# Kernel optimization log

Measured on AMD Instinct MI355X. Metric: run time of the kernel, lower is better.

Reference implementation:

```python
import jax, jax.numpy as jnp
import numpy as np
from jax.scipy.special import logsumexp

N, K, D = 131072, 256, 32


def setup_inputs() -> dict:
    key = jax.random.key(0)
    k1, k2, k3 = jax.random.split(key, 3)
    points = jax.random.normal(k1, (N, D), dtype=jnp.float32)
    centers = jax.random.uniform(k2, (K, D), dtype=jnp.float32)
    # well-conditioned inverse-sqrt covariances (original used 15*I; scaled to
    # avoid float32 overflow in sqrt(det(covs_inv)) for D=32)
    covs_inv_sqrt = (0.5 * jnp.broadcast_to(jnp.eye(D, dtype=jnp.float32), (K, D, D))
                     + 0.02 * jax.random.normal(k3, (K, D, D), dtype=jnp.float32))
    weights = jnp.ones((K,), dtype=jnp.float32)
    threshold = jnp.zeros((1,), dtype=jnp.float32)
    return {"points": points, "centers": centers,
            "covs_inv_sqrt": covs_inv_sqrt, "weights": weights,
            "threshold": threshold}


def reference(points, centers, covs_inv_sqrt, weights, threshold):
    # refresh(): equal_clusters=True branch
    w = jnp.abs(weights)
    center_prs = w / (w.sum() + 1e-30)                       # [K]
    covs_inv = jnp.einsum('kde,kfe->kdf', covs_inv_sqrt, covs_inv_sqrt)  # [K,D,D]
    coefs = center_prs * jnp.sqrt(jnp.linalg.det(covs_inv))  # [K]

    # pairwise weighted sqdist: q_ij = (x_i - c_j)^T A_j (x_i - c_j)
    B = covs_inv.reshape(K, D * D)                           # [K, D*D]
    X2 = (points[:, :, None] * points[:, None, :]).reshape(N, D * D)  # [N, D*D]
    t_xAx = X2 @ B.T                                         # [N, K]
    m = jnp.einsum('kde,ke->kd', covs_inv, centers)          # A_j c_j, [K,D]
    t_xAc = points @ m.T                                     # [N, K]
    t_cAc = jnp.einsum('kd,kd->k', m, centers)               # [K]
    d_ij = -0.5 * (t_xAx - 2.0 * t_xAc + t_cAc[None, :])     # [N, K]

    # weighted logsumexp over centers, then subtract threshold
    ll = logsumexp(d_ij, axis=1, b=coefs[None, :])           # [N]
    return ll[:, None] - threshold[0]                        # [N, 1]
```

## Files before the change

kernel.cpp:

```cpp
#include <hip/hip_runtime.h>
#include <math.h>

#define NPTS 131072
#define KCOMP 256
#define DIM 32
#define NREAL 560
#define NCH 18
#define PSIF_BYTES 294912
#define WS_NEED (PSIF_BYTES + KCOMP * 4)

typedef __attribute__((ext_vector_type(8))) short short8;
typedef __attribute__((ext_vector_type(16))) float f32x16;

__device__ __forceinline__ unsigned short f2bf(float v) {
    unsigned u = __float_as_uint(v);
    u += 0x7fffu + ((u >> 16) & 1u);
    return (unsigned short)(u >> 16);
}

__device__ __forceinline__ unsigned pkbf(float lo, float hi) {
#if __has_builtin(__builtin_amdgcn_perm)
    const unsigned a = __float_as_uint(hi) + 0x8000u;
    const unsigned b = __float_as_uint(lo) + 0x8000u;
    return __builtin_amdgcn_perm(a, b, 0x07060302u);
#else
    return (unsigned)f2bf(lo) | ((unsigned)f2bf(hi) << 16);
#endif
}

__device__ __forceinline__ void dma16(const uint4* g, uint4* s) {
    __builtin_amdgcn_global_load_lds(
        (const __attribute__((address_space(1))) void*)g,
        (__attribute__((address_space(3))) void*)s, 16, 0, 0);
}

template<int N>
__device__ __forceinline__ void waitbar() {
    if constexpr (N == 2)
        asm volatile("s_waitcnt vmcnt(2) lgkmcnt(0)\ns_barrier" ::: "memory");
    else if constexpr (N == 1)
        asm volatile("s_waitcnt vmcnt(1) lgkmcnt(0)\ns_barrier" ::: "memory");
    else
        asm volatile("s_waitcnt vmcnt(0) lgkmcnt(0)\ns_barrier" ::: "memory");
}

constexpr int PfxT(int d) { return 32 * d - (d * (d - 1)) / 2; }
constexpr int rowT(int p) { int d = 0; while (d < 31 && PfxT(d + 1) <= p) ++d; return d; }
constexpr int colT(int p) { return rowT(p) + (p - PfxT(rowT(p))); }

template<int P, int J>
__device__ __forceinline__ float genOne(const float (&x)[DIM]) {
    constexpr int p = P + J;
    if constexpr (p >= NREAL) {
        return 0.f;
    } else if constexpr (p >= 528) {
        return x[p - 528];
    } else {
        constexpr int d = rowT(p);
        constexpr int f = colT(p);
        static_assert(d >= 0 && d < 32 && f >= d && f < 32, "bad feature map");
        return x[d] * x[f];
    }
}

__global__ __launch_bounds__(256) void gmm_pre(
    const float* __restrict__ S,
    const float* __restrict__ centers,
    const float* __restrict__ weights,
    unsigned short* __restrict__ PsiF,
    float* __restrict__ kc2)
{
    __shared__ float Sl[DIM][DIM + 1];
    __shared__ float As[DIM][DIM + 1];
    __shared__ float cl[DIM], ml[DIM];
    __shared__ float red[256];

    const int k = blockIdx.x, tid = threadIdx.x;

    for (int idx = tid; idx < DIM * DIM; idx += 256)
        Sl[idx >> 5][idx & 31] = S[(size_t)k * DIM * DIM + idx];
    if (tid < DIM) cl[tid] = centers[k * DIM + tid];
    __syncthreads();

    for (int idx = tid; idx < DIM * DIM; idx += 256) {
        const int d = idx >> 5, f = idx & 31;
        float a = 0.f;
#pragma unroll
        for (int e = 0; e < DIM; ++e) a = fmaf(Sl[d][e], Sl[f][e], a);
        As[d][f] = a;
    }
    __syncthreads();

    if (tid < DIM) {
        float mv = 0.f;
#pragma unroll
        for (int f = 0; f < DIM; ++f) mv = fmaf(As[tid][f], cl[f], mv);
        ml[tid] = mv;
    }
    __syncthreads();

    for (int p = tid; p < NREAL; p += 256) {
        float val;
        if (p < 528) {
            int d = 0, pr = 0;
            while (pr + (32 - d) <= p) { pr += (32 - d); ++d; }
            const int f = d + (p - pr);
            val = (f == d) ? -0.5f * As[d][d] : -As[d][f];
        } else {
            val = ml[p - 528];
        }
        const int c = p >> 6, kk = p & 63;
        const int s = kk >> 4, qq = (kk >> 3) & 1, j = kk & 7;
        const int ct = k >> 5, ll = qq * 32 + (k & 31);
        const int g = c * 2048 + (s * 8 + ct) * 64 + ll;
        PsiF[(size_t)g * 8 + j] = f2bf(val);
    }

    red[tid] = fabsf(weights[tid]);
    __syncthreads();
    for (int off = 128; off > 0; off >>= 1) {
        if (tid < off) red[tid] += red[tid + off];
        __syncthreads();
    }
    const float wsum = red[0];

    for (int j = 0; j < DIM - 1; ++j) {
        const float inv = 1.0f / As[j][j];
        for (int idx = tid; idx < DIM * DIM; idx += 256) {
            const int r = idx >> 5, c = idx & 31;
            if (r > j && c > j)
                As[r][c] = fmaf(-As[r][j] * inv, As[j][c], As[r][c]);
        }
        __syncthreads();
    }

    if (tid < DIM) red[tid] = __logf(As[tid][tid]);
    __syncthreads();
    if (tid == 0) {
        float sl = 0.f;
        for (int j = 0; j < DIM; ++j) sl += red[j];
        float cac = 0.f;
        for (int d2 = 0; d2 < DIM; ++d2) cac = fmaf(ml[d2], cl[d2], cac);
        kc2[k] = __logf(fabsf(weights[k])) - __logf(wsum + 1e-30f)
               + 0.5f * sl - 0.5f * cac;
    }
}

template<int P>
__device__ __forceinline__ void genQuad(const float (&x)[DIM], float* v) {
    v[0] = genOne<P, 0>(x);
    v[1] = genOne<P, 1>(x);
    v[2] = genOne<P, 2>(x);
    v[3] = genOne<P, 3>(x);
}

template<int CH, int SS>
__device__ __forceinline__ void genSite(const float (&x)[DIM], uint4* base,
                                        int rbg, int r32) {
    float v[8];
    genQuad<CH * 32 + SS * 8>(x, v);
    genQuad<CH * 32 + SS * 8 + 4>(x, v + 4);
    uint4 u;
    u.x = pkbf(v[0], v[1]);
    u.y = pkbf(v[2], v[3]);
    u.z = pkbf(v[4], v[5]);
    u.w = pkbf(v[6], v[7]);
    base[(SS >> 1) * 256 + rbg * 64 + (SS & 1) * 32 + r32] = u;
}

template<int CH>
__device__ __forceinline__ void genChunk(const float (&x)[DIM], uint4* sA4,
                                         int q, int rbg, int r32) {
    uint4* base = sA4 + (CH & 1) * 512;
    if constexpr (CH < 17) {
        if (q == 0)      genSite<CH, 0>(x, base, rbg, r32);
        else if (q == 1) genSite<CH, 1>(x, base, rbg, r32);
        else if (q == 2) genSite<CH, 2>(x, base, rbg, r32);
        else             genSite<CH, 3>(x, base, rbg, r32);
    } else {
        if (q == 0)      genSite<CH, 0>(x, base, rbg, r32);
        else if (q == 1) genSite<CH, 1>(x, base, rbg, r32);
    }
}

template<int C>
__device__ __forceinline__ void doChunk(const float (&x)[DIM],
    uint4* sA4, uint4* sB4, const uint4* __restrict__ PsiF4,
    f32x16 (&acc)[2][2],
    int l, int w, int q, int rbg, int r32, int rgp, int cgp)
{

    if constexpr (C + 2 < NCH) {
        constexpr int NI = (C + 2 == 17) ? 1 : 2;
        const uint4* src = PsiF4 + (C + 2) * 1024 + w * 64 + l;
        uint4* dst = sB4 + ((C + 2) % 3) * 1024 + w * 64 + l;
#pragma unroll
        for (int i = 0; i < NI; ++i) dma16(src + i * 512, dst + i * 512);
    }

    if constexpr (C + 1 < NCH) genChunk<C + 1>(x, sA4, q, rbg, r32);

    constexpr int NS = (C < 17) ? 2 : 1;
    const uint4* aa = sA4 + (C & 1) * 512;
    const uint4* bb = sB4 + (C % 3) * 1024;
#pragma unroll
    for (int s = 0; s < NS; ++s) {
        short8 f0 = __builtin_bit_cast(short8, aa[(s * 4 + rgp * 2 + 0) * 64 + l]);
        short8 f1 = __builtin_bit_cast(short8, aa[(s * 4 + rgp * 2 + 1) * 64 + l]);
#pragma unroll
        for (int cj = 0; cj < 2; ++cj) {
            short8 psi = __builtin_bit_cast(short8, bb[(s * 8 + cgp * 2 + cj) * 64 + l]);
            acc[0][cj] = __builtin_amdgcn_mfma_f32_32x32x16_bf16(psi, f0, acc[0][cj], 0, 0, 0);
            acc[1][cj] = __builtin_amdgcn_mfma_f32_32x32x16_bf16(psi, f1, acc[1][cj], 0, 0, 0);
        }
    }

    if constexpr (C <= 14)      waitbar<2>();
    else if constexpr (C == 15) waitbar<1>();
    else if constexpr (C == 16) waitbar<0>();
}

__global__ __launch_bounds__(512, 4) void gmm_mfma(
    const float* __restrict__ points,
    const unsigned short* __restrict__ PsiF,
    const float* __restrict__ kc2,
    const float* __restrict__ thr,
    float* __restrict__ out)
{
    __shared__ uint4 sA4[1024];
    __shared__ uint4 sB4[3072];
    float (*sM)[4] = (float (*)[4])sA4;
    float (*sS)[4] = (float (*)[4])(sA4 + 128);

    const int t = threadIdx.x;
    const int w = t >> 6, l = t & 63;
    const int row = t & 127, q = t >> 7;
    const int rbg = row >> 5, r32 = row & 31;
    const int rgp = w >> 2, cgp = w & 3;

    const uint4* PsiF4 = (const uint4*)PsiF;

    {
        const uint4* src = PsiF4 + w * 64 + l;
        uint4* dst = sB4 + w * 64 + l;
        dma16(src,        dst);
        dma16(src +  512, dst +  512);
        dma16(src + 1024, dst + 1024);
        dma16(src + 1536, dst + 1536);
    }

    float x[DIM];
    const float4* px = (const float4*)(points + ((size_t)blockIdx.x * 128 + row) * DIM);
#pragma unroll
    for (int j2 = 0; j2 < 8; ++j2) {
        float4 v = px[j2];
        x[4 * j2 + 0] = v.x; x[4 * j2 + 1] = v.y;
        x[4 * j2 + 2] = v.z; x[4 * j2 + 3] = v.w;
    }

    f32x16 acc[2][2];
#pragma unroll
    for (int ri = 0; ri < 2; ++ri)
#pragma unroll
        for (int cj = 0; cj < 2; ++cj)
#pragma unroll
            for (int r = 0; r < 16; ++r) acc[ri][cj][r] = 0.f;

    genChunk<0>(x, sA4, q, rbg, r32);
    __syncthreads();

    doChunk<0>(x, sA4, sB4, PsiF4, acc, l, w, q, rbg, r32, rgp, cgp);
    doChunk<1>(x, sA4, sB4, PsiF4, acc, l, w, q, rbg, r32, rgp, cgp);
    doChunk<2>(x, sA4, sB4, PsiF4, acc, l, w, q, rbg, r32, rgp, cgp);
    doChunk<3>(x, sA4, sB4, PsiF4, acc, l, w, q, rbg, r32, rgp, cgp);
    doChunk<4>(x, sA4, sB4, PsiF4, acc, l, w, q, rbg, r32, rgp, cgp);
    doChunk<5>(x, sA4, sB4, PsiF4, acc, l, w, q, rbg, r32, rgp, cgp);
    doChunk<6>(x, sA4, sB4, PsiF4, acc, l, w, q, rbg, r32, rgp, cgp);
    doChunk<7>(x, sA4, sB4, PsiF4, acc, l, w, q, rbg, r32, rgp, cgp);
    doChunk<8>(x, sA4, sB4, PsiF4, acc, l, w, q, rbg, r32, rgp, cgp);
    doChunk<9>(x, sA4, sB4, PsiF4, acc, l, w, q, rbg, r32, rgp, cgp);
    doChunk<10>(x, sA4, sB4, PsiF4, acc, l, w, q, rbg, r32, rgp, cgp);
    doChunk<11>(x, sA4, sB4, PsiF4, acc, l, w, q, rbg, r32, rgp, cgp);
    doChunk<12>(x, sA4, sB4, PsiF4, acc, l, w, q, rbg, r32, rgp, cgp);
    doChunk<13>(x, sA4, sB4, PsiF4, acc, l, w, q, rbg, r32, rgp, cgp);
    doChunk<14>(x, sA4, sB4, PsiF4, acc, l, w, q, rbg, r32, rgp, cgp);
    doChunk<15>(x, sA4, sB4, PsiF4, acc, l, w, q, rbg, r32, rgp, cgp);
    doChunk<16>(x, sA4, sB4, PsiF4, acc, l, w, q, rbg, r32, rgp, cgp);
    doChunk<17>(x, sA4, sB4, PsiF4, acc, l, w, q, rbg, r32, rgp, cgp);

    const int hi = l >> 5;
    float mr[2] = { -INFINITY, -INFINITY };
#pragma unroll
    for (int cj = 0; cj < 2; ++cj) {
        const float* kp = kc2 + (cgp * 2 + cj) * 32 + 4 * hi;
        const float4 q0 = *(const float4*)(kp);
        const float4 q1 = *(const float4*)(kp + 8);
        const float4 q2 = *(const float4*)(kp + 16);
        const float4 q3 = *(const float4*)(kp + 24);
#pragma unroll
        for (int ri = 0; ri < 2; ++ri) {
#define KADD(R, QC) { float _v = acc[ri][cj][R] + (QC); acc[ri][cj][R] = _v; mr[ri] = fmaxf(mr[ri], _v); }
            KADD(0, q0.x)  KADD(1, q0.y)  KADD(2, q0.z)  KADD(3, q0.w)
            KADD(4, q1.x)  KADD(5, q1.y)  KADD(6, q1.z)  KADD(7, q1.w)
            KADD(8, q2.x)  KADD(9, q2.y)  KADD(10, q2.z) KADD(11, q2.w)
            KADD(12, q3.x) KADD(13, q3.y) KADD(14, q3.z) KADD(15, q3.w)
#undef KADD
        }
    }
#pragma unroll
    for (int ri = 0; ri < 2; ++ri) {
        float m = fmaxf(mr[ri], __shfl_xor(mr[ri], 32, 64));
        float sv = 0.f;
#pragma unroll
        for (int cj = 0; cj < 2; ++cj)
#pragma unroll
            for (int rg = 0; rg < 16; ++rg)
                sv += __expf(acc[ri][cj][rg] - m);
        sv += __shfl_xor(sv, 32, 64);
        if (l < 32) {
            sM[(rgp * 2 + ri) * 32 + l][cgp] = m;
            sS[(rgp * 2 + ri) * 32 + l][cgp] = sv;
        }
    }
    __syncthreads();

    if (t < 128) {
        const float m0 = sM[t][0], m1 = sM[t][1], m2 = sM[t][2], m3 = sM[t][3];
        const float M = fmaxf(fmaxf(m0, m1), fmaxf(m2, m3));
        const float Sv = sS[t][0] * __expf(m0 - M) + sS[t][1] * __expf(m1 - M)
                       + sS[t][2] * __expf(m2 - M) + sS[t][3] * __expf(m3 - M);
        out[(size_t)blockIdx.x * 128 + t] = M + __logf(Sv) - thr[0];
    }
}

extern "C" void kernel_launch(void* const* d_in, const int* in_sizes, int n_in,
                              void* d_out, int out_size, void* d_ws, size_t ws_size,
                              hipStream_t stream) {
    const float* points  = (const float*)d_in[0];
    const float* centers = (const float*)d_in[1];
    const float* covs    = (const float*)d_in[2];
    const float* weights = (const float*)d_in[3];
    const float* thr     = (const float*)d_in[4];
    float* out = (float*)d_out;

    unsigned short* PsiF = (unsigned short*)d_ws;
    float* kc2 = (float*)((char*)d_ws + PSIF_BYTES);

    gmm_pre<<<KCOMP, 256, 0, stream>>>(covs, centers, weights, PsiF, kc2);
    gmm_mfma<<<NPTS / 128, 512, 0, stream>>>(points, PsiF, kc2, thr, out);
}
```

Baseline: 130.2 us.

## Load Psi fragments directly into registers and shrink blocks to 64 points

```diff
diff --git a/kernel.cpp b/kernel.cpp
--- a/kernel.cpp
+++ b/kernel.cpp
@@ -28,20 +28,8 @@
 #endif
 }
 
-__device__ __forceinline__ void dma16(const uint4* g, uint4* s) {
-    __builtin_amdgcn_global_load_lds(
-        (const __attribute__((address_space(1))) void*)g,
-        (__attribute__((address_space(3))) void*)s, 16, 0, 0);
-}
-
-template<int N>
-__device__ __forceinline__ void waitbar() {
-    if constexpr (N == 2)
-        asm volatile("s_waitcnt vmcnt(2) lgkmcnt(0)\ns_barrier" ::: "memory");
-    else if constexpr (N == 1)
-        asm volatile("s_waitcnt vmcnt(1) lgkmcnt(0)\ns_barrier" ::: "memory");
-    else
-        asm volatile("s_waitcnt vmcnt(0) lgkmcnt(0)\ns_barrier" ::: "memory");
+__device__ __forceinline__ void barrier_lds() {
+    asm volatile("s_waitcnt lgkmcnt(0)\ns_barrier" ::: "memory");
 }
 
 constexpr int PfxT(int d) { return 32 * d - (d * (d - 1)) / 2; }
@@ -155,8 +143,7 @@
 }
 
 template<int CH, int SS>
-__device__ __forceinline__ void genSite(const float (&x)[DIM], uint4* base,
-                                        int rbg, int r32) {
+__device__ __forceinline__ void genSiteW(const float (&x)[DIM], uint4* sA4, int l) {
     float v[8];
     genQuad<CH * 32 + SS * 8>(x, v);
     genQuad<CH * 32 + SS * 8 + 4>(x, v + 4);
@@ -165,92 +152,82 @@
     u.y = pkbf(v[2], v[3]);
     u.z = pkbf(v[4], v[5]);
     u.w = pkbf(v[6], v[7]);
-    base[(SS >> 1) * 256 + rbg * 64 + (SS & 1) * 32 + r32] = u;
+    uint4* base = sA4 + (CH & 1) * 256;
+    base[(((SS >> 1) * 2 + (l >> 5)) << 6) + (SS & 1) * 32 + (l & 31)] = u;
 }
 
 template<int CH>
-__device__ __forceinline__ void genChunk(const float (&x)[DIM], uint4* sA4,
-                                         int q, int rbg, int r32) {
-    uint4* base = sA4 + (CH & 1) * 512;
+__device__ __forceinline__ void genChunkW(const float (&x)[DIM], uint4* sA4,
+                                          int w, int l) {
     if constexpr (CH < 17) {
-        if (q == 0)      genSite<CH, 0>(x, base, rbg, r32);
-        else if (q == 1) genSite<CH, 1>(x, base, rbg, r32);
-        else if (q == 2) genSite<CH, 2>(x, base, rbg, r32);
-        else             genSite<CH, 3>(x, base, rbg, r32);
+        if      (w == 0) genSiteW<CH, 0>(x, sA4, l);
+        else if (w == 1) genSiteW<CH, 1>(x, sA4, l);
+        else if (w == 2) genSiteW<CH, 2>(x, sA4, l);
+        else             genSiteW<CH, 3>(x, sA4, l);
     } else {
-        if (q == 0)      genSite<CH, 0>(x, base, rbg, r32);
-        else if (q == 1) genSite<CH, 1>(x, base, rbg, r32);
+        if      (w == 0) genSiteW<CH, 0>(x, sA4, l);
+        else if (w == 1) genSiteW<CH, 1>(x, sA4, l);
+    }
+}
+
+template<int C>
+__device__ __forceinline__ void loadB(const uint4* __restrict__ PsiF4,
+                                      uint4 (&st)[4], int l, int cgp) {
+    const uint4* p = PsiF4 + C * 1024 + (cgp * 2) * 64 + l;
+    st[0] = p[0];
+    st[1] = p[64];
+    if constexpr (C < 17) {
+        st[2] = p[512];
+        st[3] = p[512 + 64];
     }
 }
 
 template<int C>
 __device__ __forceinline__ void doChunk(const float (&x)[DIM],
-    uint4* sA4, uint4* sB4, const uint4* __restrict__ PsiF4,
-    f32x16 (&acc)[2][2],
-    int l, int w, int q, int rbg, int r32, int rgp, int cgp)
+    uint4* sA4, const uint4* __restrict__ PsiF4,
+    uint4 (&cur)[4], uint4 (&nxt)[4],
+    f32x16 (&acc)[2][2], int l, int w)
 {
 
-    if constexpr (C + 2 < NCH) {
-        constexpr int NI = (C + 2 == 17) ? 1 : 2;
-        const uint4* src = PsiF4 + (C + 2) * 1024 + w * 64 + l;
-        uint4* dst = sB4 + ((C + 2) % 3) * 1024 + w * 64 + l;
-#pragma unroll
-        for (int i = 0; i < NI; ++i) dma16(src + i * 512, dst + i * 512);
-    }
-
-    if constexpr (C + 1 < NCH) genChunk<C + 1>(x, sA4, q, rbg, r32);
+    if constexpr (C + 1 < NCH) loadB<C + 1>(PsiF4, nxt, l, w);
+
+    if constexpr (C + 1 < NCH) genChunkW<C + 1>(x, sA4, w, l);
 
     constexpr int NS = (C < 17) ? 2 : 1;
-    const uint4* aa = sA4 + (C & 1) * 512;
-    const uint4* bb = sB4 + (C % 3) * 1024;
-#pragma unroll
-    for (int s = 0; s < NS; ++s) {
-        short8 f0 = __builtin_bit_cast(short8, aa[(s * 4 + rgp * 2 + 0) * 64 + l]);
-        short8 f1 = __builtin_bit_cast(short8, aa[(s * 4 + rgp * 2 + 1) * 64 + l]);
+    const uint4* aa = sA4 + (C & 1) * 256;
+#pragma unroll
+    for (int s2 = 0; s2 < NS; ++s2) {
+        short8 f0 = __builtin_bit_cast(short8, aa[(s2 * 2 + 0) * 64 + l]);
+        short8 f1 = __builtin_bit_cast(short8, aa[(s2 * 2 + 1) * 64 + l]);
 #pragma unroll
         for (int cj = 0; cj < 2; ++cj) {
-            short8 psi = __builtin_bit_cast(short8, bb[(s * 8 + cgp * 2 + cj) * 64 + l]);
+            short8 psi = __builtin_bit_cast(short8, cur[s2 * 2 + cj]);
             acc[0][cj] = __builtin_amdgcn_mfma_f32_32x32x16_bf16(psi, f0, acc[0][cj], 0, 0, 0);
             acc[1][cj] = __builtin_amdgcn_mfma_f32_32x32x16_bf16(psi, f1, acc[1][cj], 0, 0, 0);
         }
     }
 
-    if constexpr (C <= 14)      waitbar<2>();
-    else if constexpr (C == 15) waitbar<1>();
-    else if constexpr (C == 16) waitbar<0>();
-}
-
-__global__ __launch_bounds__(512, 4) void gmm_mfma(
+    if constexpr (C + 1 < NCH) barrier_lds();
+}
+
+__global__ __launch_bounds__(256, 3) void gmm_mfma(
     const float* __restrict__ points,
     const unsigned short* __restrict__ PsiF,
     const float* __restrict__ kc2,
     const float* __restrict__ thr,
     float* __restrict__ out)
 {
-    __shared__ uint4 sA4[1024];
-    __shared__ uint4 sB4[3072];
-    float (*sM)[4] = (float (*)[4])sA4;
-    float (*sS)[4] = (float (*)[4])(sA4 + 128);
+    __shared__ uint4 sA4[512];
+    __shared__ float sM[64][4];
+    __shared__ float sS[64][4];
 
     const int t = threadIdx.x;
     const int w = t >> 6, l = t & 63;
-    const int row = t & 127, q = t >> 7;
-    const int rbg = row >> 5, r32 = row & 31;
-    const int rgp = w >> 2, cgp = w & 3;
 
     const uint4* PsiF4 = (const uint4*)PsiF;
 
-    {
-        const uint4* src = PsiF4 + w * 64 + l;
-        uint4* dst = sB4 + w * 64 + l;
-        dma16(src,        dst);
-        dma16(src +  512, dst +  512);
-        dma16(src + 1024, dst + 1024);
-        dma16(src + 1536, dst + 1536);
-    }
-
     float x[DIM];
-    const float4* px = (const float4*)(points + ((size_t)blockIdx.x * 128 + row) * DIM);
+    const float4* px = (const float4*)(points + ((size_t)blockIdx.x * 64 + l) * DIM);
 #pragma unroll
     for (int j2 = 0; j2 < 8; ++j2) {
         float4 v = px[j2];
@@ -266,33 +243,36 @@
 #pragma unroll
             for (int r = 0; r < 16; ++r) acc[ri][cj][r] = 0.f;
 
-    genChunk<0>(x, sA4, q, rbg, r32);
-    __syncthreads();
-
-    doChunk<0>(x, sA4, sB4, PsiF4, acc, l, w, q, rbg, r32, rgp, cgp);
-    doChunk<1>(x, sA4, sB4, PsiF4, acc, l, w, q, rbg, r32, rgp, cgp);
-    doChunk<2>(x, sA4, sB4, PsiF4, acc, l, w, q, rbg, r32, rgp, cgp);
-    doChunk<3>(x, sA4, sB4, PsiF4, acc, l, w, q, rbg, r32, rgp, cgp);
-    doChunk<4>(x, sA4, sB4, PsiF4, acc, l, w, q, rbg, r32, rgp, cgp);
-    doChunk<5>(x, sA4, sB4, PsiF4, acc, l, w, q, rbg, r32, rgp, cgp);
-    doChunk<6>(x, sA4, sB4, PsiF4, acc, l, w, q, rbg, r32, rgp, cgp);
-    doChunk<7>(x, sA4, sB4, PsiF4, acc, l, w, q, rbg, r32, rgp, cgp);
-    doChunk<8>(x, sA4, sB4, PsiF4, acc, l, w, q, rbg, r32, rgp, cgp);
-    doChunk<9>(x, sA4, sB4, PsiF4, acc, l, w, q, rbg, r32, rgp, cgp);
-    doChunk<10>(x, sA4, sB4, PsiF4, acc, l, w, q, rbg, r32, rgp, cgp);
-    doChunk<11>(x, sA4, sB4, PsiF4, acc, l, w, q, rbg, r32, rgp, cgp);
-    doChunk<12>(x, sA4, sB4, PsiF4, acc, l, w, q, rbg, r32, rgp, cgp);
-    doChunk<13>(x, sA4, sB4, PsiF4, acc, l, w, q, rbg, r32, rgp, cgp);
-    doChunk<14>(x, sA4, sB4, PsiF4, acc, l, w, q, rbg, r32, rgp, cgp);
-    doChunk<15>(x, sA4, sB4, PsiF4, acc, l, w, q, rbg, r32, rgp, cgp);
-    doChunk<16>(x, sA4, sB4, PsiF4, acc, l, w, q, rbg, r32, rgp, cgp);
-    doChunk<17>(x, sA4, sB4, PsiF4, acc, l, w, q, rbg, r32, rgp, cgp);
+    uint4 stA[4], stB[4];
+    loadB<0>(PsiF4, stA, l, w);
+
+    genChunkW<0>(x, sA4, w, l);
+    barrier_lds();
+
+    doChunk<0>(x, sA4, PsiF4, stA, stB, acc, l, w);
+    doChunk<1>(x, sA4, PsiF4, stB, stA, acc, l, w);
+    doChunk<2>(x, sA4, PsiF4, stA, stB, acc, l, w);
+    doChunk<3>(x, sA4, PsiF4, stB, stA, acc, l, w);
+    doChunk<4>(x, sA4, PsiF4, stA, stB, acc, l, w);
+    doChunk<5>(x, sA4, PsiF4, stB, stA, acc, l, w);
+    doChunk<6>(x, sA4, PsiF4, stA, stB, acc, l, w);
+    doChunk<7>(x, sA4, PsiF4, stB, stA, acc, l, w);
+    doChunk<8>(x, sA4, PsiF4, stA, stB, acc, l, w);
+    doChunk<9>(x, sA4, PsiF4, stB, stA, acc, l, w);
+    doChunk<10>(x, sA4, PsiF4, stA, stB, acc, l, w);
+    doChunk<11>(x, sA4, PsiF4, stB, stA, acc, l, w);
+    doChunk<12>(x, sA4, PsiF4, stA, stB, acc, l, w);
+    doChunk<13>(x, sA4, PsiF4, stB, stA, acc, l, w);
+    doChunk<14>(x, sA4, PsiF4, stA, stB, acc, l, w);
+    doChunk<15>(x, sA4, PsiF4, stB, stA, acc, l, w);
+    doChunk<16>(x, sA4, PsiF4, stA, stB, acc, l, w);
+    doChunk<17>(x, sA4, PsiF4, stB, stA, acc, l, w);
 
     const int hi = l >> 5;
     float mr[2] = { -INFINITY, -INFINITY };
 #pragma unroll
     for (int cj = 0; cj < 2; ++cj) {
-        const float* kp = kc2 + (cgp * 2 + cj) * 32 + 4 * hi;
+        const float* kp = kc2 + (w * 2 + cj) * 32 + 4 * hi;
         const float4 q0 = *(const float4*)(kp);
         const float4 q1 = *(const float4*)(kp + 8);
         const float4 q2 = *(const float4*)(kp + 16);
@@ -318,18 +298,18 @@
                 sv += __expf(acc[ri][cj][rg] - m);
         sv += __shfl_xor(sv, 32, 64);
         if (l < 32) {
-            sM[(rgp * 2 + ri) * 32 + l][cgp] = m;
-            sS[(rgp * 2 + ri) * 32 + l][cgp] = sv;
-        }
-    }
-    __syncthreads();
-
-    if (t < 128) {
+            sM[ri * 32 + l][w] = m;
+            sS[ri * 32 + l][w] = sv;
+        }
+    }
+    __syncthreads();
+
+    if (t < 64) {
         const float m0 = sM[t][0], m1 = sM[t][1], m2 = sM[t][2], m3 = sM[t][3];
         const float M = fmaxf(fmaxf(m0, m1), fmaxf(m2, m3));
         const float Sv = sS[t][0] * __expf(m0 - M) + sS[t][1] * __expf(m1 - M)
                        + sS[t][2] * __expf(m2 - M) + sS[t][3] * __expf(m3 - M);
-        out[(size_t)blockIdx.x * 128 + t] = M + __logf(Sv) - thr[0];
+        out[(size_t)blockIdx.x * 64 + t] = M + __logf(Sv) - thr[0];
     }
 }
 
@@ -347,5 +327,5 @@
     float* kc2 = (float*)((char*)d_ws + PSIF_BYTES);
 
     gmm_pre<<<KCOMP, 256, 0, stream>>>(covs, centers, weights, PsiF, kc2);
-    gmm_mfma<<<NPTS / 128, 512, 0, stream>>>(points, PsiF, kc2, thr, out);
-}
+    gmm_mfma<<<NPTS / 64, 256, 0, stream>>>(points, PsiF, kc2, thr, out);
+}
```

Measured after the change: 130.7 us. About the same (+0.4%).
